# Performance work log

Measured on AMD Instinct MI355X. Metric: run time of the kernel, lower is better.

## Reference

```python
import jax, jax.numpy as jnp
import numpy as np

N = 50000      # nodes
E = 800000     # edges (before self-loops)
IN_CH = 5
HID = 32
HEADS = 4
NEG_SLOPE = 0.2  # PyG GATConv default


def _gat_layer(x, src, dst, W, att_src, att_dst, bias, concat):
    """PyG GATConv (eval mode). W: [F_in, H*C], att_*: [H, C], bias matches output."""
    H, C = att_src.shape
    h = (x @ W).reshape(-1, H, C)                       # [N, H, C]
    a_src = jnp.sum(h * att_src, axis=-1)               # [N, H]
    a_dst = jnp.sum(h * att_dst, axis=-1)               # [N, H]
    e = jax.nn.leaky_relu(a_src[src] + a_dst[dst], negative_slope=NEG_SLOPE)  # [E', H]
    m = jax.ops.segment_max(e, dst, num_segments=N)     # stable softmax per dst segment
    ex = jnp.exp(e - m[dst])
    denom = jax.ops.segment_sum(ex, dst, num_segments=N)
    alpha = ex / denom[dst]                             # [E', H]
    out = jax.ops.segment_sum(alpha[:, :, None] * h[src], dst, num_segments=N)  # [N, H, C]
    out = out.reshape(N, H * C) if concat else out.mean(axis=1)
    return out + bias


def setup_inputs() -> dict:
    key = jax.random.key(0)
    ks = jax.random.split(key, 14)
    g = lambda k, shape, s=0.1: (jax.random.normal(k, shape, jnp.float32) * s)
    return {
        "x": jax.random.normal(ks[0], (N, IN_CH), jnp.float32),
        "edge_index": jax.random.randint(ks[1], (2, E), 0, N, jnp.int32),
        "W1": g(ks[2], (IN_CH, HEADS * HID)),
        "att_src1": g(ks[3], (HEADS, HID)),
        "att_dst1": g(ks[4], (HEADS, HID)),
        "b1": jnp.zeros((HEADS * HID,), jnp.float32),
        "W2": g(ks[5], (HEADS * HID, HID)),
        "att_src2": g(ks[6], (1, HID)),
        "att_dst2": g(ks[7], (1, HID)),
        "b2": jnp.zeros((HID,), jnp.float32),
        "Wc1": g(ks[8], (HID, 16)),
        "bc1": jnp.zeros((16,), jnp.float32),
        "Wc2": g(ks[9], (16, 1)),
        "bc2": jnp.zeros((1,), jnp.float32),
    }


def reference(x, edge_index, W1, att_src1, att_dst1, b1, W2, att_src2, att_dst2, b2, Wc1, bc1, Wc2, bc2):
    # add self loops (PyG GATConv default add_self_loops=True)
    loops = jnp.arange(N, dtype=edge_index.dtype)
    src = jnp.concatenate([edge_index[0], loops])
    dst = jnp.concatenate([edge_index[1], loops])
    # dropout layers are identity in eval mode
    h = jax.nn.elu(_gat_layer(x, src, dst, W1, att_src1, att_dst1, b1, concat=True))
    h = jax.nn.elu(_gat_layer(h, src, dst, W2, att_src2, att_dst2, b2, concat=False))
    h = jax.nn.relu(h @ Wc1 + bc1)
    out = (h @ Wc2 + bc2)[:, 0]   # squeeze(-1) -> [N]
    return out
```

## Files before the change

kernel.cpp:

```cpp
#include <hip/hip_runtime.h>
#include <hip/hip_fp16.h>

#define NEG_SLOPE 0.2f
#define BSHIFT 6
#define SCATB 256

__device__ __forceinline__ float elu1(float v) { return v > 0.f ? v : expm1f(v); }
__device__ __forceinline__ float lrelu(float v) { return v > 0.f ? v : NEG_SLOPE * v; }

__device__ __forceinline__ int ge_off(const int* __restrict__ blkoff,
                                      const int* __restrict__ bsum2, int j) {
    if (j == 0) return 0;
    int b = (j - 1) >> 8;
    int v = blkoff[j];
    if (b >= 1) v += bsum2[b - 1];
    return v;
}


__global__ __launch_bounds__(256) void k_cnt_attn(
    const int* __restrict__ ei, int E, int ET, int chunk,
    int* __restrict__ Cmat, int nbuck,
    const float* __restrict__ x, const float* __restrict__ W1,
    const float* __restrict__ att_s, const float* __restrict__ att_d,
    __half* __restrict__ rech, float4* __restrict__ ad4f, int N) {
    __shared__ int hist[784];
    __shared__ float Ps[5][4], Pd[5][4];
    if (blockIdx.x < SCATB) {
        for (int i = threadIdx.x; i < nbuck; i += 256) hist[i] = 0;
        __syncthreads();
        int k = blockIdx.x;
        int e0 = k * chunk, e1 = min(e0 + chunk, ET);
        for (int e = e0 + threadIdx.x; e < e1; e += 256) {
            int d = (e < E) ? ei[E + e] : e - E;
            atomicAdd(&hist[d >> BSHIFT], 1);
        }
        __syncthreads();
        for (int i = threadIdx.x; i < nbuck; i += 256)
            Cmat[i * SCATB + k] = hist[i];
    } else {
        if (threadIdx.x < 40) {
            int pair = threadIdx.x & 1, idx = threadIdx.x >> 1;
            int k = idx >> 2, h = idx & 3;
            const float* att = pair ? att_d : att_s;
            float r = 0.f;
#pragma unroll
            for (int c = 0; c < 32; ++c) r = fmaf(W1[k * 128 + h * 32 + c], att[h * 32 + c], r);
            if (pair) Pd[k][h] = r; else Ps[k][h] = r;
        }
        __syncthreads();
        int n = (blockIdx.x - SCATB) * 256 + threadIdx.x;
        if (n >= N) return;
        float xv[5];
#pragma unroll
        for (int k = 0; k < 5; ++k) xv[k] = x[(size_t)n * 5 + k];
        float s0 = 0, s1 = 0, s2 = 0, s3 = 0, d0 = 0, d1 = 0, d2 = 0, d3 = 0;
#pragma unroll
        for (int k = 0; k < 5; ++k) {
            s0 = fmaf(xv[k], Ps[k][0], s0); s1 = fmaf(xv[k], Ps[k][1], s1);
            s2 = fmaf(xv[k], Ps[k][2], s2); s3 = fmaf(xv[k], Ps[k][3], s3);
            d0 = fmaf(xv[k], Pd[k][0], d0); d1 = fmaf(xv[k], Pd[k][1], d1);
            d2 = fmaf(xv[k], Pd[k][2], d2); d3 = fmaf(xv[k], Pd[k][3], d3);
        }
        __half2 a[4], b[4];
        a[0] = __floats2half2_rn(s0, s1);
        a[1] = __floats2half2_rn(s2, s3);
        a[2] = __floats2half2_rn(xv[0], xv[1]);
        a[3] = __floats2half2_rn(xv[2], xv[3]);
        b[0] = __floats2half2_rn(xv[4], 0.f);
        b[1] = b[2] = b[3] = __floats2half2_rn(0.f, 0.f);
        *(float4*)(rech + (size_t)n * 16)     = *(float4*)a;
        *(float4*)(rech + (size_t)n * 16 + 8) = *(float4*)b;
        ad4f[n] = make_float4(d0, d1, d2, d3);
    }
}

__global__ __launch_bounds__(256) void k_scan1(
    const int* __restrict__ Cmat, int* __restrict__ blkoff, int* __restrict__ bsum, int M) {
    __shared__ int ws4[4], wsoff[4];
    int i = blockIdx.x * 256 + threadIdx.x;
    int lane = threadIdx.x & 63, w = threadIdx.x >> 6;
    int v = (i < M) ? Cmat[i] : 0;
    int sc = v;
#pragma unroll
    for (int m = 1; m < 64; m <<= 1) {
        int t = __shfl_up(sc, m, 64);
        if (lane >= m) sc += t;
    }
    if (lane == 63) ws4[w] = sc;
    __syncthreads();
    if (threadIdx.x == 0) {
        int r = 0;
#pragma unroll
        for (int j = 0; j < 4; ++j) { wsoff[j] = r; r += ws4[j]; }
        bsum[blockIdx.x] = r;
    }
    __syncthreads();
    if (i < M) blkoff[i + 1] = sc + wsoff[w];
    if (i == 0) blkoff[0] = 0;
}

__global__ __launch_bounds__(1024) void k_scan2(
    int* __restrict__ bsum, int nb, int* __restrict__ off, int N, int ET) {
    __shared__ int wsum[16];
    int i = threadIdx.x, lane = i & 63, w = i >> 6;
    if (i == 0) off[N] = ET;
    int v = (i < nb) ? bsum[i] : 0, sc = v;
#pragma unroll
    for (int m = 1; m < 64; m <<= 1) {
        int t = __shfl_up(sc, m, 64);
        if (lane >= m) sc += t;
    }
    if (lane == 63) wsum[w] = sc;
    __syncthreads();
    if (w == 0 && lane < 16) {
        int s2 = wsum[lane];
#pragma unroll
        for (int m = 1; m < 16; m <<= 1) {
            int t = __shfl_up(s2, m, 16);
            if (lane >= m) s2 += t;
        }
        wsum[lane] = s2;
    }
    __syncthreads();
    int carry = (w == 0) ? 0 : wsum[w - 1];
    if (i < nb) bsum[i] = carry + sc;
}

__global__ __launch_bounds__(256) void k_scat(
    const int* __restrict__ ei, int E, int ET, int chunk,
    const int* __restrict__ blkoff, const int* __restrict__ bsum2,
    unsigned* __restrict__ pairs, int nbuck) {
    __shared__ int cur[784];
    int k = blockIdx.x;
    for (int i = threadIdx.x; i < nbuck; i += 256)
        cur[i] = ge_off(blkoff, bsum2, i * SCATB + k);
    __syncthreads();
    int e0 = k * chunk, e1 = min(e0 + chunk, ET);
    for (int e = e0 + threadIdx.x; e < e1; e += 256) {
        int s, d;
        if (e < E) { s = ei[e]; d = ei[E + e]; } else { s = d = e - E; }
        int p = atomicAdd(&cur[d >> BSHIFT], 1);
        pairs[p] = (unsigned)s | ((unsigned)(d & 63) << 16);
    }
}

__global__ __launch_bounds__(256) void k_sortB(
    const unsigned* __restrict__ pairs, const int* __restrict__ blkoff,
    const int* __restrict__ bsum2, int* __restrict__ off,
    int* __restrict__ csr_src, int N, int ET, int nbuck) {
    __shared__ int hist[64], cur[64];
    __shared__ unsigned pl[1536];
    int b = blockIdx.x;
    int base = ge_off(blkoff, bsum2, b * SCATB);
    int end  = (b + 1 < nbuck) ? ge_off(blkoff, bsum2, (b + 1) * SCATB) : ET;
    int cnt = end - base;
    int stg = min(cnt, 1536);
    int dstBase = b << BSHIFT;
    if (threadIdx.x < 64) hist[threadIdx.x] = 0;
    for (int i = threadIdx.x; i < stg; i += 256) pl[i] = pairs[base + i];
    __syncthreads();
    for (int i = threadIdx.x; i < cnt; i += 256) {
        unsigned pr = (i < stg) ? pl[i] : pairs[base + i];
        atomicAdd(&hist[pr >> 16], 1);
    }
    __syncthreads();
    if (threadIdx.x < 64) {
        int v = hist[threadIdx.x], sc = v;
#pragma unroll
        for (int m = 1; m < 64; m <<= 1) {
            int t = __shfl_up(sc, m, 64);
            if (threadIdx.x >= m) sc += t;
        }
        int ex = sc - v;
        cur[threadIdx.x] = ex;
        int d = dstBase + threadIdx.x;
        if (d < N) off[d] = base + ex;
    }
    __syncthreads();
    for (int i = threadIdx.x; i < cnt; i += 256) {
        unsigned pr = (i < stg) ? pl[i] : pairs[base + i];
        int r = atomicAdd(&cur[pr >> 16], 1);
        csr_src[base + r] = (int)(pr & 0xFFFFu);
    }
}


__global__ __launch_bounds__(256) void k_agg1(
    const int* __restrict__ off, const int* __restrict__ csr_src,
    const __half* __restrict__ rech, const float4* __restrict__ ad4f,
    const float* __restrict__ W1, const float* __restrict__ b1,
    __half* __restrict__ out1h, int N) {
    __shared__ float Wl[5 * 128];
    __shared__ float b1l[128];
    for (int i = threadIdx.x; i < 5 * 128; i += 256) Wl[i] = W1[i];
    if (threadIdx.x < 128) b1l[threadIdx.x] = b1[threadIdx.x];
    __syncthreads();
    int g = (blockIdx.x * 256 + threadIdx.x) >> 4;
    int lane = threadIdx.x & 15;
    if (g >= N) return;
    int p0 = off[g], p1 = off[g + 1];
    float4 ad = ad4f[g];
    float den0 = 0, den1 = 0, den2 = 0, den3 = 0;
    float acc[4][5] = {};
    for (int p = p0 + lane; p < p1; p += 16) {
        int s = csr_src[p];
        const __half* r = rech + (size_t)s * 16;
        float4 q = *(const float4*)r;
        const __half2* hp = (const __half2*)&q;
        float2 as01 = __half22float2(hp[0]);
        float2 as23 = __half22float2(hp[1]);
        float2 x01  = __half22float2(hp[2]);
        float2 x23  = __half22float2(hp[3]);
        float  x4   = __half2float(r[8]);
        float v0 = __expf(lrelu(as01.x + ad.x));
        float v1 = __expf(lrelu(as01.y + ad.y));
        float v2 = __expf(lrelu(as23.x + ad.z));
        float v3 = __expf(lrelu(as23.y + ad.w));
        den0 += v0; den1 += v1; den2 += v2; den3 += v3;
        float xk[5] = {x01.x, x01.y, x23.x, x23.y, x4};
#pragma unroll
        for (int k = 0; k < 5; ++k) {
            acc[0][k] = fmaf(v0, xk[k], acc[0][k]);
            acc[1][k] = fmaf(v1, xk[k], acc[1][k]);
            acc[2][k] = fmaf(v2, xk[k], acc[2][k]);
            acc[3][k] = fmaf(v3, xk[k], acc[3][k]);
        }
    }
#pragma unroll
    for (int m = 8; m; m >>= 1) {
        den0 += __shfl_xor(den0, m, 16); den1 += __shfl_xor(den1, m, 16);
        den2 += __shfl_xor(den2, m, 16); den3 += __shfl_xor(den3, m, 16);
#pragma unroll
        for (int h = 0; h < 4; ++h)
#pragma unroll
            for (int k = 0; k < 5; ++k) acc[h][k] += __shfl_xor(acc[h][k], m, 16);
    }
    int c0 = lane * 8;
    int h = lane >> 2;
    float dh = (h == 0) ? den0 : (h == 1) ? den1 : (h == 2) ? den2 : den3;
    float ih = 1.f / dh;
    float ag[5];
#pragma unroll
    for (int k = 0; k < 5; ++k) ag[k] = acc[h][k] * ih;
    __half2 ph[4];
#pragma unroll
    for (int j = 0; j < 4; ++j) {
        int c = c0 + 2 * j;
        float rr = b1l[c];
#pragma unroll
        for (int k = 0; k < 5; ++k) rr = fmaf(ag[k], Wl[k * 128 + c], rr);
        float oa = elu1(rr);
        rr = b1l[c + 1];
#pragma unroll
        for (int k = 0; k < 5; ++k) rr = fmaf(ag[k], Wl[k * 128 + c + 1], rr);
        float ob = elu1(rr);
        ph[j] = __floats2half2_rn(oa, ob);
    }
    *(float4*)(out1h + (size_t)g * 128 + c0) = *(float4*)ph;
}


__global__ __launch_bounds__(256) void k_feat2(
    const __half* __restrict__ out1h, const float* __restrict__ W2,
    const float* __restrict__ att_s, const float* __restrict__ att_d,
    __half* __restrict__ h2h, float* __restrict__ a_s, float* __restrict__ a_d, int N) {
    __shared__ __half Wt[32 * 132];
    for (int i = threadIdx.x; i < 4096; i += 256) {
        int k = i >> 5, c = i & 31;
        Wt[c * 132 + k] = __float2half_rn(W2[i]);
    }
    __syncthreads();
    int t = blockIdx.x * 256 + threadIdx.x;
    int n = t >> 5, c = t & 31;
    if (n >= N) return;
    const float4* hr4 = (const float4*)(out1h + (size_t)n * 128);
    const __half2* wrow = (const __half2*)(Wt + c * 132);
    float acc = 0.f;
#pragma unroll
    for (int k4 = 0; k4 < 16; ++k4) {
        float4 q = hr4[k4];
        const __half2* hp = (const __half2*)&q;
#pragma unroll
        for (int m = 0; m < 4; ++m) {
            float2 f  = __half22float2(hp[m]);
            float2 wv = __half22float2(wrow[k4 * 4 + m]);
            acc = fmaf(f.x, wv.x, acc);
            acc = fmaf(f.y, wv.y, acc);
        }
    }
    h2h[(size_t)n * 32 + c] = __float2half_rn(acc);
    float as = acc * att_s[c], ad = acc * att_d[c];
#pragma unroll
    for (int m = 16; m; m >>= 1) {
        as += __shfl_xor(as, m, 32);
        ad += __shfl_xor(ad, m, 32);
    }
    if (c == 0) { a_s[n] = as; a_d[n] = ad; }
}

__global__ __launch_bounds__(256) void k_agg2h(
    const int* __restrict__ off, const int* __restrict__ csr_src,
    const float* __restrict__ a_s, const float* __restrict__ a_d,
    const __half* __restrict__ h2h, const float* __restrict__ b2,
    const float* __restrict__ Wc1, const float* __restrict__ bc1,
    const float* __restrict__ Wc2, const float* __restrict__ bc2,
    float* __restrict__ out, int N) {
    __shared__ float Wl[512];
    __shared__ float b2l[32], b1l[16], w2l[16];
    for (int i = threadIdx.x; i < 512; i += 256) Wl[i] = Wc1[i];
    if (threadIdx.x < 32) b2l[threadIdx.x] = b2[threadIdx.x];
    if (threadIdx.x < 16) {
        b1l[threadIdx.x] = bc1[threadIdx.x];
        w2l[threadIdx.x] = Wc2[threadIdx.x];
    }
    __syncthreads();
    int g = (blockIdx.x * 256 + threadIdx.x) >> 5;
    int lane = threadIdx.x & 31;
    if (g >= N) return;
    int p0 = off[g], p1 = off[g + 1];
    float ad = a_d[g];
    float acc = 0.f, den = 0.f;
    for (int base = p0; base < p1; base += 32) {
        int rem = p1 - base;
        int s = g;
        float w = 0.f;
        if (lane < rem) {
            s = csr_src[base + lane];
            w = __expf(lrelu(a_s[s] + ad));
        }
        den += w;
        int cnt = min(rem, 32);
        int rc = (cnt + 7) & ~7;
        for (int j = 0; j < rc; j += 8) {
#pragma unroll
            for (int jj = 0; jj < 8; ++jj) {
                int   sj = __shfl(s, j + jj, 32);
                float wj = __shfl(w, j + jj, 32);
                float hv = __half2float(h2h[(size_t)sj * 32 + lane]);
                acc = fmaf(wj, hv, acc);
            }
        }
    }
#pragma unroll
    for (int m = 16; m; m >>= 1) den += __shfl_xor(den, m, 32);
    float z = elu1(fmaf(acc, 1.f / den, b2l[lane]));
    float y = b1l[lane & 15];
#pragma unroll
    for (int c = 0; c < 32; ++c) {
        float zc = __shfl(z, c, 32);
        y = fmaf(zc, Wl[c * 16 + (lane & 15)], y);
    }
    y = fmaxf(y, 0.f);
    float t = (lane < 16) ? y * w2l[lane] : 0.f;
#pragma unroll
    for (int m = 8; m; m >>= 1) t += __shfl_xor(t, m, 32);
    if (lane == 0) out[g] = t + bc2[0];
}

extern "C" void kernel_launch(void* const* d_in, const int* in_sizes, int n_in,
                              void* d_out, int out_size, void* d_ws, size_t ws_size,
                              hipStream_t stream) {
    const float* x   = (const float*)d_in[0];
    const int*   ei  = (const int*)d_in[1];
    const float* W1  = (const float*)d_in[2];
    const float* as1 = (const float*)d_in[3];
    const float* ad1 = (const float*)d_in[4];
    const float* b1  = (const float*)d_in[5];
    const float* W2  = (const float*)d_in[6];
    const float* as2 = (const float*)d_in[7];
    const float* ad2 = (const float*)d_in[8];
    const float* b2  = (const float*)d_in[9];
    const float* Wc1 = (const float*)d_in[10];
    const float* bc1 = (const float*)d_in[11];
    const float* Wc2 = (const float*)d_in[12];
    const float* bc2 = (const float*)d_in[13];
    float* out = (float*)d_out;

    const int N = out_size;
    const int E = in_sizes[1] / 2;
    const int ET = E + N;
    const int nbuck = (N + 63) >> BSHIFT;
    const int M = nbuck * SCATB;
    const int chunk = (ET + SCATB - 1) / SCATB;

    auto cdiv = [](long long a, long long b) { return (int)((a + b - 1) / b); };
    const int B = 256;
    const int NB2 = cdiv(M, B);
    const int nAttn = cdiv(N, B);

    float*    ws    = (float*)d_ws;
    __half*   out1h = (__half*)ws;
    __half*   h2h   = (__half*)(ws + (size_t)N * 64);
    __half*   rech  = (__half*)(ws + (size_t)N * 80);
    float4*   ad4f  = (float4*)(ws + (size_t)N * 88);
    float*    a_s2  = ws + (size_t)N * 92;
    float*    a_d2  = a_s2 + N;
    int*      off   = (int*)(a_d2 + N);
    int*      csr_src = off + (N + 2);
    int*      Cmat  = csr_src + ET;
    int*      blkoff = Cmat + M;
    int*      bsum  = blkoff + (M + 2);
    unsigned* pairs = (unsigned*)(bsum + 1024);

    k_cnt_attn<<<SCATB + nAttn, B, 0, stream>>>(ei, E, ET, chunk, Cmat, nbuck,
                                                x, W1, as1, ad1, rech, ad4f, N);
    k_scan1<<<NB2, B, 0, stream>>>(Cmat, blkoff, bsum, M);
    k_scan2<<<1, 1024, 0, stream>>>(bsum, NB2, off, N, ET);
    k_scat<<<SCATB, B, 0, stream>>>(ei, E, ET, chunk, blkoff, bsum, pairs, nbuck);
    k_sortB<<<nbuck, B, 0, stream>>>(pairs, blkoff, bsum, off, csr_src, N, ET, nbuck);

    k_agg1<<<cdiv((long long)N * 16, B), B, 0, stream>>>(off, csr_src, rech, ad4f,
                                                         W1, b1, out1h, N);

    k_feat2<<<cdiv((long long)N * 32, B), B, 0, stream>>>(out1h, W2, as2, ad2, h2h,
                                                          a_s2, a_d2, N);
    k_agg2h<<<cdiv((long long)N * 32, B), B, 0, stream>>>(off, csr_src, a_s2, a_d2, h2h, b2,
                                                          Wc1, bc1, Wc2, bc2, out, N);
}
```

Before: 113.4 us.

## Fuse scan kernels with last-block pattern, narrow agg1 groups, stage agg2 weights in LDS

Merges the two-level scan into one kernel: each block publishes its sum, and the last block to finish, found through an atomic counter reset earlier in the count kernel, scans the block totals. This removes one kernel launch. k_agg1 now uses 8 lanes per node instead of 16, halving the thread count, and each lane writes 16 output channels. k_agg2h reads (src, weight) pairs from shared memory with vector loads instead of issuing two shuffles per edge. The last-block scan relies on correct atomic and fence ordering, and the narrower agg1 groups give less parallelism per node.

New measurement: 171.0 us. 50.8% more time.

```diff
diff --git a/kernel.cpp b/kernel.cpp
--- a/kernel.cpp
+++ b/kernel.cpp
@@ -23,7 +23,8 @@
     int* __restrict__ Cmat, int nbuck,
     const float* __restrict__ x, const float* __restrict__ W1,
     const float* __restrict__ att_s, const float* __restrict__ att_d,
-    __half* __restrict__ rech, float4* __restrict__ ad4f, int N) {
+    __half* __restrict__ rech, float4* __restrict__ ad4f, int N,
+    int* __restrict__ done) {
     __shared__ int hist[784];
     __shared__ float Ps[5][4], Pd[5][4];
     if (blockIdx.x < SCATB) {
@@ -39,6 +40,7 @@
         for (int i = threadIdx.x; i < nbuck; i += 256)
             Cmat[i * SCATB + k] = hist[i];
     } else {
+        if (blockIdx.x == SCATB && threadIdx.x == 0) *done = 0;
         if (threadIdx.x < 40) {
             int pair = threadIdx.x & 1, idx = threadIdx.x >> 1;
             int k = idx >> 2, h = idx & 3;
@@ -75,9 +77,11 @@
     }
 }
 
-__global__ __launch_bounds__(256) void k_scan1(
-    const int* __restrict__ Cmat, int* __restrict__ blkoff, int* __restrict__ bsum, int M) {
+__global__ __launch_bounds__(256) void k_scan1f(
+    const int* __restrict__ Cmat, int* __restrict__ blkoff, int* __restrict__ bsum,
+    int M, int* __restrict__ done, int* __restrict__ off, int N, int ET) {
     __shared__ int ws4[4], wsoff[4];
+    __shared__ int lastDone;
     int i = blockIdx.x * 256 + threadIdx.x;
     int lane = threadIdx.x & 63, w = threadIdx.x >> 6;
     int v = (i < M) ? Cmat[i] : 0;
@@ -93,38 +97,49 @@
         int r = 0;
 #pragma unroll
         for (int j = 0; j < 4; ++j) { wsoff[j] = r; r += ws4[j]; }
-        bsum[blockIdx.x] = r;
+        __hip_atomic_store(&bsum[blockIdx.x], r, __ATOMIC_RELEASE, __HIP_MEMORY_SCOPE_AGENT);
     }
     __syncthreads();
     if (i < M) blkoff[i + 1] = sc + wsoff[w];
-    if (i == 0) blkoff[0] = 0;
-}
-
-__global__ __launch_bounds__(1024) void k_scan2(
-    int* __restrict__ bsum, int nb, int* __restrict__ off, int N, int ET) {
-    __shared__ int wsum[16];
-    int i = threadIdx.x, lane = i & 63, w = i >> 6;
-    if (i == 0) off[N] = ET;
-    int v = (i < nb) ? bsum[i] : 0, sc = v;
+    if (i == 0) { blkoff[0] = 0; off[N] = ET; }
+    __threadfence();
+    if (threadIdx.x == 0)
+        lastDone = (__hip_atomic_fetch_add(done, 1, __ATOMIC_ACQ_REL,
+                                           __HIP_MEMORY_SCOPE_AGENT) == (int)gridDim.x - 1);
+    __syncthreads();
+    if (!lastDone) return;
+    int nb = gridDim.x;
+    int t = threadIdx.x;
+    int vv[4], ssum = 0;
+#pragma unroll
+    for (int j = 0; j < 4; ++j) {
+        int idx = t * 4 + j;
+        vv[j] = (idx < nb) ? __hip_atomic_load(&bsum[idx], __ATOMIC_RELAXED,
+                                               __HIP_MEMORY_SCOPE_AGENT) : 0;
+        ssum += vv[j];
+    }
+    int sc2 = ssum;
 #pragma unroll
     for (int m = 1; m < 64; m <<= 1) {
-        int t = __shfl_up(sc, m, 64);
-        if (lane >= m) sc += t;
-    }
-    if (lane == 63) wsum[w] = sc;
-    __syncthreads();
-    if (w == 0 && lane < 16) {
-        int s2 = wsum[lane];
-#pragma unroll
-        for (int m = 1; m < 16; m <<= 1) {
-            int t = __shfl_up(s2, m, 16);
-            if (lane >= m) s2 += t;
-        }
-        wsum[lane] = s2;
-    }
-    __syncthreads();
-    int carry = (w == 0) ? 0 : wsum[w - 1];
-    if (i < nb) bsum[i] = carry + sc;
+        int u = __shfl_up(sc2, m, 64);
+        if (lane >= m) sc2 += u;
+    }
+    __syncthreads();
+    if (lane == 63) ws4[w] = sc2;
+    __syncthreads();
+    if (threadIdx.x == 0) {
+        int r = 0;
+#pragma unroll
+        for (int j = 0; j < 4; ++j) { wsoff[j] = r; r += ws4[j]; }
+    }
+    __syncthreads();
+    int run = sc2 - ssum + wsoff[w];
+#pragma unroll
+    for (int j = 0; j < 4; ++j) {
+        int idx = t * 4 + j;
+        run += vv[j];
+        if (idx < nb) bsum[idx] = run;
+    }
 }
 
 __global__ __launch_bounds__(256) void k_scat(
@@ -196,14 +211,14 @@
     for (int i = threadIdx.x; i < 5 * 128; i += 256) Wl[i] = W1[i];
     if (threadIdx.x < 128) b1l[threadIdx.x] = b1[threadIdx.x];
     __syncthreads();
-    int g = (blockIdx.x * 256 + threadIdx.x) >> 4;
-    int lane = threadIdx.x & 15;
+    int g = (blockIdx.x * 256 + threadIdx.x) >> 3;
+    int lane = threadIdx.x & 7;
     if (g >= N) return;
     int p0 = off[g], p1 = off[g + 1];
     float4 ad = ad4f[g];
     float den0 = 0, den1 = 0, den2 = 0, den3 = 0;
     float acc[4][5] = {};
-    for (int p = p0 + lane; p < p1; p += 16) {
+    for (int p = p0 + lane; p < p1; p += 8) {
         int s = csr_src[p];
         const __half* r = rech + (size_t)s * 16;
         float4 q = *(const float4*)r;
@@ -228,24 +243,28 @@
         }
     }
 #pragma unroll
-    for (int m = 8; m; m >>= 1) {
-        den0 += __shfl_xor(den0, m, 16); den1 += __shfl_xor(den1, m, 16);
-        den2 += __shfl_xor(den2, m, 16); den3 += __shfl_xor(den3, m, 16);
+    for (int m = 4; m; m >>= 1) {
+        den0 += __shfl_xor(den0, m, 8); den1 += __shfl_xor(den1, m, 8);
+        den2 += __shfl_xor(den2, m, 8); den3 += __shfl_xor(den3, m, 8);
 #pragma unroll
         for (int h = 0; h < 4; ++h)
 #pragma unroll
-            for (int k = 0; k < 5; ++k) acc[h][k] += __shfl_xor(acc[h][k], m, 16);
-    }
-    int c0 = lane * 8;
-    int h = lane >> 2;
+            for (int k = 0; k < 5; ++k) acc[h][k] += __shfl_xor(acc[h][k], m, 8);
+    }
+    int h = lane >> 1;
     float dh = (h == 0) ? den0 : (h == 1) ? den1 : (h == 2) ? den2 : den3;
     float ih = 1.f / dh;
     float ag[5];
 #pragma unroll
-    for (int k = 0; k < 5; ++k) ag[k] = acc[h][k] * ih;
-    __half2 ph[4];
-#pragma unroll
-    for (int j = 0; j < 4; ++j) {
+    for (int k = 0; k < 5; ++k) {
+        float av = (h == 0) ? acc[0][k] : (h == 1) ? acc[1][k]
+                 : (h == 2) ? acc[2][k] : acc[3][k];
+        ag[k] = av * ih;
+    }
+    int c0 = lane * 16;
+    __half2 ph[8];
+#pragma unroll
+    for (int j = 0; j < 8; ++j) {
         int c = c0 + 2 * j;
         float rr = b1l[c];
 #pragma unroll
@@ -257,7 +276,9 @@
         float ob = elu1(rr);
         ph[j] = __floats2half2_rn(oa, ob);
     }
-    *(float4*)(out1h + (size_t)g * 128 + c0) = *(float4*)ph;
+    float4* op = (float4*)(out1h + (size_t)g * 128 + c0);
+    op[0] = ((float4*)ph)[0];
+    op[1] = ((float4*)ph)[1];
 }
 
 
@@ -308,6 +329,7 @@
     float* __restrict__ out, int N) {
     __shared__ float Wl[512];
     __shared__ float b2l[32], b1l[16], w2l[16];
+    __shared__ uint2 wsb[256];
     for (int i = threadIdx.x; i < 512; i += 256) Wl[i] = Wc1[i];
     if (threadIdx.x < 32) b2l[threadIdx.x] = b2[threadIdx.x];
     if (threadIdx.x < 16) {
@@ -317,10 +339,12 @@
     __syncthreads();
     int g = (blockIdx.x * 256 + threadIdx.x) >> 5;
     int lane = threadIdx.x & 31;
+    int gl = threadIdx.x >> 5;
     if (g >= N) return;
     int p0 = off[g], p1 = off[g + 1];
     float ad = a_d[g];
     float acc = 0.f, den = 0.f;
+    const uint4* wp = (const uint4*)(wsb + (gl << 5));
     for (int base = p0; base < p1; base += 32) {
         int rem = p1 - base;
         int s = g;
@@ -330,15 +354,19 @@
             w = __expf(lrelu(a_s[s] + ad));
         }
         den += w;
+        wsb[threadIdx.x] = make_uint2((unsigned)s, __float_as_uint(w));
         int cnt = min(rem, 32);
         int rc = (cnt + 7) & ~7;
         for (int j = 0; j < rc; j += 8) {
 #pragma unroll
-            for (int jj = 0; jj < 8; ++jj) {
-                int   sj = __shfl(s, j + jj, 32);
-                float wj = __shfl(w, j + jj, 32);
-                float hv = __half2float(h2h[(size_t)sj * 32 + lane]);
-                acc = fmaf(wj, hv, acc);
+            for (int jj = 0; jj < 4; ++jj) {
+                uint4 q = wp[(j >> 1) + jj];
+                float w0 = __uint_as_float(q.y);
+                float w1 = __uint_as_float(q.w);
+                float h0 = __half2float(h2h[(size_t)q.x * 32 + lane]);
+                float h1 = __half2float(h2h[(size_t)q.z * 32 + lane]);
+                acc = fmaf(w0, h0, acc);
+                acc = fmaf(w1, h1, acc);
             }
         }
     }
@@ -401,17 +429,17 @@
     int*      Cmat  = csr_src + ET;
     int*      blkoff = Cmat + M;
     int*      bsum  = blkoff + (M + 2);
-    unsigned* pairs = (unsigned*)(bsum + 1024);
+    int*      done  = bsum + 1024;
+    unsigned* pairs = (unsigned*)(done + 4);
 
     k_cnt_attn<<<SCATB + nAttn, B, 0, stream>>>(ei, E, ET, chunk, Cmat, nbuck,
-                                                x, W1, as1, ad1, rech, ad4f, N);
-    k_scan1<<<NB2, B, 0, stream>>>(Cmat, blkoff, bsum, M);
-    k_scan2<<<1, 1024, 0, stream>>>(bsum, NB2, off, N, ET);
+                                                x, W1, as1, ad1, rech, ad4f, N, done);
+    k_scan1f<<<NB2, B, 0, stream>>>(Cmat, blkoff, bsum, M, done, off, N, ET);
     k_scat<<<SCATB, B, 0, stream>>>(ei, E, ET, chunk, blkoff, bsum, pairs, nbuck);
     k_sortB<<<nbuck, B, 0, stream>>>(pairs, blkoff, bsum, off, csr_src, N, ET, nbuck);
 
-    k_agg1<<<cdiv((long long)N * 16, B), B, 0, stream>>>(off, csr_src, rech, ad4f,
-                                                         W1, b1, out1h, N);
+    k_agg1<<<cdiv((long long)N * 8, B), B, 0, stream>>>(off, csr_src, rech, ad4f,
+                                                        W1, b1, out1h, N);
 
     k_feat2<<<cdiv((long long)N * 32, B), B, 0, stream>>>(out1h, W2, as2, ad2, h2h,
                                                           a_s2, a_d2, N);
```
